# Performance work log

Measured on AMD Instinct MI355X. Metric: run time of the kernel, lower is better.

## Reference

```python
import jax, jax.numpy as jnp
import numpy as np

GRID = 128            # hardcoded in NeRFRenderer.__init__
BOUND = 4.0           # cfg.bound
CASCADE = 3           # 1 + ceil(log2(BOUND))
N_CELLS = GRID ** 3
N_CAMS = 32


def _part1by2(x):
    # interleave bits of a 10-bit int with two zero bits (instant-ngp morton3D)
    x = x & 0x000003FF
    x = (x | (x << 16)) & 0x030000FF
    x = (x | (x << 8)) & 0x0300F00F
    x = (x | (x << 4)) & 0x030C30C3
    x = (x | (x << 2)) & 0x09249249
    return x


def _morton3d(coords):
    # coords: [N,3] int32 -> [N] int32 morton codes (x lowest bit)
    x = _part1by2(coords[:, 0])
    y = _part1by2(coords[:, 1])
    z = _part1by2(coords[:, 2])
    return x | (y << 1) | (z << 2)


def setup_inputs() -> dict:
    key = jax.random.key(0)
    k1, k2 = jax.random.split(key)
    density_grid = jax.random.uniform(k1, (CASCADE, N_CELLS), dtype=jnp.float32)
    poses = jax.random.normal(k2, (N_CAMS, 4, 4), dtype=jnp.float32)
    # fx, fy, cx, cy for a 512x512 pinhole camera
    intrinsics = jnp.array([1111.1, 1111.1, 256.0, 256.0], dtype=jnp.float32)
    return {"density_grid": density_grid, "poses": poses, "intrinsics": intrinsics}


def reference(density_grid, poses, intrinsics):
    # Faithful vectorized mark_untrained_grid: for every grid cell and cascade,
    # test aabb containment and visibility in any camera frustum, then scatter
    # -1 into density_grid at the morton-encoded cell index where untrained.
    fx, fy, cx, cy = intrinsics[0], intrinsics[1], intrinsics[2], intrinsics[3]
    g = jnp.arange(GRID, dtype=jnp.int32)
    xx, yy, zz = jnp.meshgrid(g, g, g, indexing="ij")
    coords = jnp.stack([xx.ravel(), yy.ravel(), zz.ravel()], axis=-1)  # [N,3]
    indices = _morton3d(coords)                                        # [N] permutation of 0..N-1
    world = 2.0 * coords.astype(jnp.float32) / (GRID - 1) - 1.0        # [N,3] in [-1,1]

    R = poses[:, :3, :3]   # [B,3,3]
    t = poses[:, :3, 3]    # [B,3]

    new_grid = []
    for cas in range(CASCADE):
        bnd = min(2.0 ** cas, BOUND)
        h = bnd / GRID                       # half_grid_size
        cxyz = world * (bnd - h)             # [N,3] cascade world coords

        in_aabb = jnp.all(cxyz >= (-BOUND - h), axis=-1) & \
                  jnp.all(cxyz <= (BOUND + h), axis=-1)          # [N]

        # cam_xyzs = (cxyz - t[b]) @ R[b]  -> [B,N,3]
        cam = jnp.einsum("nj,bjk->bnk", cxyz, R) - jnp.einsum("bj,bjk->bk", t, R)[:, None, :]
        mask_z = cam[..., 2] > 0
        mask_x = jnp.abs(cam[..., 0]) < (cx / fx) * cam[..., 2] + 2.0 * h
        mask_y = jnp.abs(cam[..., 1]) < (cy / fy) * cam[..., 2] + 2.0 * h
        visible = jnp.any(mask_z & mask_x & mask_y, axis=0)      # [N]

        untrained = (~in_aabb) | (~visible)                      # [N] in coord order
        mark = jnp.zeros((N_CELLS,), dtype=bool).at[indices].set(untrained)  # morton scatter
        new_grid.append(jnp.where(mark, jnp.float32(-1.0), density_grid[cas]))

    return jnp.stack(new_grid, axis=0)
```

## Files before the change

kernel.cpp:

```cpp
#include <hip/hip_runtime.h>
#include <stdint.h>


constexpr int GRIDN  = 128;
constexpr int NCELLS = GRIDN * GRIDN * GRIDN;
constexpr int NCAMS  = 32;
constexpr int BLOCK  = 256;
constexpr int CPB    = BLOCK * 8;

__device__ __forceinline__ uint32_t compact1by2(uint32_t x) {
    x &= 0x09249249u;
    x = (x ^ (x >> 2))  & 0x030c30c3u;
    x = (x ^ (x >> 4))  & 0x0300f00fu;
    x = (x ^ (x >> 8))  & 0x030000ffu;
    x = (x ^ (x >> 16)) & 0x000003ffu;
    return x;
}

__launch_bounds__(BLOCK)
__global__ void nerf_mark_kernel(const float* __restrict__ dg,
                                 const float* __restrict__ poses,
                                 const float* __restrict__ intr,
                                 float* __restrict__ out) {
    __shared__ __align__(16) float sRd[NCAMS * 12];
    __shared__ float sc0[GRIDN];
    __shared__ float sax[2];

    constexpr float S0  = 1.0f - 1.0f / 128.0f;
    constexpr float T0  = 2.0f / 128.0f, T1 = 4.0f / 128.0f, T2 = 8.0f / 128.0f;
    constexpr float PAD = 1e-3f;

    const int tid = threadIdx.x;
    for (int i = tid; i < NCAMS * 12; i += BLOCK) {
        int b = i / 12, k = i - b * 12;
        const float* P = poses + b * 16;
        if (k < 9) {
            sRd[i] = P[(k / 3) * 4 + (k % 3)];
        } else {
            int kk = k - 9;
            sRd[i] = fmaf(P[11], P[8 + kk], fmaf(P[7], P[4 + kk], P[3] * P[kk]));
        }
    }
    if (tid < GRIDN) {
        float w = (2.0f * (float)tid) / 127.0f - 1.0f;
        sc0[tid] = __fmul_rn(w, S0);
    }
    if (tid == 0) { sax[0] = intr[2] / intr[0]; sax[1] = intr[3] / intr[1]; }
    __syncthreads();

    const int lane = tid & 63;
    const uint32_t wbase = (uint32_t)blockIdx.x * CPB + ((uint32_t)(tid >> 6)) * 512u;

    const int xi = ((lane & 1) << 1) | (((lane >> 3) & 1) << 2);
    const int yi = (((lane >> 1) & 1) << 1) | (((lane >> 4) & 1) << 2);
    const int zi = (((lane >> 2) & 1) << 1) | (((lane >> 5) & 1) << 2);
    const int X0 = compact1by2(wbase);
    const int Y0 = compact1by2(wbase >> 1);
    const int Z0 = compact1by2(wbase >> 2);
    const float cxv[2] = { sc0[X0 + xi], sc0[X0 + xi + 1] };
    const float cyv[2] = { sc0[Y0 + yi], sc0[Y0 + yi + 1] };
    const float czv[2] = { sc0[Z0 + zi], sc0[Z0 + zi + 1] };
    const float ax = sax[0], ay = sax[1];

    const float gxl = sc0[X0], gxh = sc0[X0 + 7];
    const float gyl = sc0[Y0], gyh = sc0[Y0 + 7];
    const float gzl = sc0[Z0], gzh = sc0[Z0 + 7];
    const float gcx = 0.5f * (gxl + gxh), ghx = 0.5f * (gxh - gxl);
    const float gcy = 0.5f * (gyl + gyh), ghy = 0.5f * (gyh - gyl);
    const float gcz = 0.5f * (gzl + gzh), ghz = 0.5f * (gzh - gzl);

    const int cb = lane & 31;
    bool po0, in0, po1, in1, po2, in2;
    {
        const float4* A = reinterpret_cast<const float4*>(&sRd[cb * 12]);
        const float4 qa = A[0], qb = A[1], qc = A[2];
        const float ddx = qc.y, ddy = qc.z, ddz = qc.w;
        const float pcx = fmaf(gcz, qb.z, fmaf(gcy, qa.w, gcx * qa.x));
        const float pcy = fmaf(gcz, qb.w, fmaf(gcy, qb.x, gcx * qa.y));
        const float pcz = fmaf(gcz, qc.x, fmaf(gcy, qb.y, gcx * qa.z));
        const float F1 = fmaf(ax, pcz, -pcx), F2 = fmaf(ax, pcz, pcx);
        const float F3 = fmaf(ay, pcz, -pcy), F4 = fmaf(ay, pcz, pcy);
        const float r0 = fmaf(ghz, fabsf(qc.x), fmaf(ghy, fabsf(qb.y), ghx * fabsf(qa.z)));
        const float a1x = fmaf(ax, qa.z, -qa.x), a1y = fmaf(ax, qb.y, -qa.w), a1z = fmaf(ax, qc.x, -qb.z);
        const float a2x = fmaf(ax, qa.z,  qa.x), a2y = fmaf(ax, qb.y,  qa.w), a2z = fmaf(ax, qc.x,  qb.z);
        const float a3x = fmaf(ay, qa.z, -qa.y), a3y = fmaf(ay, qb.y, -qb.x), a3z = fmaf(ay, qc.x, -qb.w);
        const float a4x = fmaf(ay, qa.z,  qa.y), a4y = fmaf(ay, qb.y,  qb.x), a4z = fmaf(ay, qc.x,  qb.w);
        const float r1 = fmaf(ghz, fabsf(a1z), fmaf(ghy, fabsf(a1y), ghx * fabsf(a1x)));
        const float r2 = fmaf(ghz, fabsf(a2z), fmaf(ghy, fabsf(a2y), ghx * fabsf(a2x)));
        const float r3 = fmaf(ghz, fabsf(a3z), fmaf(ghy, fabsf(a3y), ghx * fabsf(a3x)));
        const float r4 = fmaf(ghz, fabsf(a4z), fmaf(ghy, fabsf(a4y), ghx * fabsf(a4x)));
        const float e1 = fmaf(ax, ddz, -ddx), e2 = fmaf(ax, ddz, ddx);
        const float e3 = fmaf(ay, ddz, -ddy), e4 = fmaf(ay, ddz, ddy);

        auto classify = [&](float s, float T, bool& poss, bool& allin) {
            const float v0 = fmaf(s, pcz, -ddz);
            const float v1 = fmaf(s, F1, T - e1);
            const float v2 = fmaf(s, F2, T - e2);
            const float v3 = fmaf(s, F3, T - e3);
            const float v4 = fmaf(s, F4, T - e4);
            const float m0h = fmaf(s, r0, v0), m0l = fmaf(-s, r0, v0);
            const float m1h = fmaf(s, r1, v1), m1l = fmaf(-s, r1, v1);
            const float m2h = fmaf(s, r2, v2), m2l = fmaf(-s, r2, v2);
            const float m3h = fmaf(s, r3, v3), m3l = fmaf(-s, r3, v3);
            const float m4h = fmaf(s, r4, v4), m4l = fmaf(-s, r4, v4);
            poss  = !((m0h <= -PAD) | (m1h <= -PAD) | (m2h <= -PAD)
                                    | (m3h <= -PAD) | (m4h <= -PAD));
            allin = (m0l >= PAD) & (m1l >= PAD) & (m2l >= PAD)
                                 & (m3l >= PAD) & (m4l >= PAD);
        };
        classify(1.0f, T0, po0, in0);
        classify(2.0f, T1, po1, in1);
        classify(4.0f, T2, po2, in2);
    }

    const uint32_t allin0 = (uint32_t)__ballot(in0);
    const uint32_t allin1 = (uint32_t)__ballot(in1);
    const uint32_t allin2 = (uint32_t)__ballot(in2);
    const uint32_t poss0  = (uint32_t)__ballot(po0);
    const uint32_t poss1  = (uint32_t)__ballot(po1);
    const uint32_t poss2  = (uint32_t)__ballot(po2);

    const bool sat0 = (allin0 != 0u), sat1 = (allin1 != 0u), sat2 = (allin2 != 0u);
    bool v0[8], v1[8], v2[8];
    #pragma unroll
    for (int s = 0; s < 8; ++s) { v0[s] = sat0; v1[s] = sat1; v2[s] = sat2; }

    const uint32_t u0 = sat0 ? 0u : poss0;
    const uint32_t u1 = sat1 ? 0u : poss1;
    const uint32_t u2 = sat2 ? 0u : poss2;
    uint32_t u = u0 | u1 | u2;
    while (u) {
        const int b = __ffs(u) - 1;
        const uint32_t bit = 1u << b;
        u &= u - 1;
        const float4* B = reinterpret_cast<const float4*>(&sRd[b * 12]);
        const float4 qa = B[0], qb = B[1], qc = B[2];

        float p0[8], p1[8], p2[8];
        #pragma unroll
        for (int x = 0; x < 2; ++x) {
            const float i0 = cxv[x] * qa.x;
            const float i1 = cxv[x] * qa.y;
            const float i2 = cxv[x] * qa.z;
            #pragma unroll
            for (int y = 0; y < 2; ++y) {
                const float j0 = fmaf(cyv[y], qa.w, i0);
                const float j1 = fmaf(cyv[y], qb.x, i1);
                const float j2 = fmaf(cyv[y], qb.y, i2);
                #pragma unroll
                for (int z = 0; z < 2; ++z) {
                    const int s = x + 2 * y + 4 * z;
                    p0[s] = fmaf(czv[z], qb.z, j0);
                    p1[s] = fmaf(czv[z], qb.w, j1);
                    p2[s] = fmaf(czv[z], qc.x, j2);
                }
            }
        }

        if (u0 & bit) {
            #pragma unroll
            for (int s = 0; s < 8; ++s) {
                const float zz = __fsub_rn(p2[s], qc.w);
                const float xx = __fsub_rn(p0[s], qc.y);
                const float yy = __fsub_rn(p1[s], qc.z);
                v0[s] = v0[s] | ((zz > 0.0f)
                              & (fabsf(xx) < __fadd_rn(__fmul_rn(ax, zz), T0))
                              & (fabsf(yy) < __fadd_rn(__fmul_rn(ay, zz), T0)));
            }
        }
        if (u1 & bit) {
            #pragma unroll
            for (int s = 0; s < 8; ++s) {
                const float zz = fmaf(2.0f, p2[s], -qc.w);
                const float xx = fmaf(2.0f, p0[s], -qc.y);
                const float yy = fmaf(2.0f, p1[s], -qc.z);
                v1[s] = v1[s] | ((zz > 0.0f)
                              & (fabsf(xx) < __fadd_rn(__fmul_rn(ax, zz), T1))
                              & (fabsf(yy) < __fadd_rn(__fmul_rn(ay, zz), T1)));
            }
        }
        if (u2 & bit) {
            #pragma unroll
            for (int s = 0; s < 8; ++s) {
                const float zz = fmaf(4.0f, p2[s], -qc.w);
                const float xx = fmaf(4.0f, p0[s], -qc.y);
                const float yy = fmaf(4.0f, p1[s], -qc.z);
                v2[s] = v2[s] | ((zz > 0.0f)
                              & (fabsf(xx) < __fadd_rn(__fmul_rn(ax, zz), T2))
                              & (fabsf(yy) < __fadd_rn(__fmul_rn(ay, zz), T2)));
            }
        }

        bool allv = true;
        #pragma unroll
        for (int s = 0; s < 8; ++s) allv = allv & v0[s] & v1[s] & v2[s];
        if (__all(allv)) break;
    }

    const int mA = (int)(wbase + 8u * (uint32_t)lane);
    #pragma unroll
    for (int cas = 0; cas < 3; ++cas) {
        const bool* v = (cas == 0) ? v0 : (cas == 1) ? v1 : v2;
        const float* src = dg + cas * NCELLS + mA;
        float* dst = out + cas * NCELLS + mA;
        const float4 dlo = *reinterpret_cast<const float4*>(src);
        const float4 dhi = *reinterpret_cast<const float4*>(src + 4);
        float4 olo, ohi;
        olo.x = v[0] ? dlo.x : -1.0f; olo.y = v[1] ? dlo.y : -1.0f;
        olo.z = v[2] ? dlo.z : -1.0f; olo.w = v[3] ? dlo.w : -1.0f;
        ohi.x = v[4] ? dhi.x : -1.0f; ohi.y = v[5] ? dhi.y : -1.0f;
        ohi.z = v[6] ? dhi.z : -1.0f; ohi.w = v[7] ? dhi.w : -1.0f;
        *reinterpret_cast<float4*>(dst)     = olo;
        *reinterpret_cast<float4*>(dst + 4) = ohi;
    }
}

extern "C" void kernel_launch(void* const* d_in, const int* in_sizes, int n_in,
                              void* d_out, int out_size, void* d_ws, size_t ws_size,
                              hipStream_t stream) {
    const float* dg    = (const float*)d_in[0];
    const float* poses = (const float*)d_in[1];
    const float* intr  = (const float*)d_in[2];
    float* out = (float*)d_out;

    nerf_mark_kernel<<<NCELLS / CPB, BLOCK, 0, stream>>>(dg, poses, intr, out);
}
```

Baseline: 15.74 us.

## Process 16 cells per thread with per-cascade early exit and skip reads for fully-untrained waves

Doubles the cells per thread to 16 (4x2x2 sub-block) and halves the grid, so the wave-level frustum culling covers 16x8x8 bricks. Visibility flags become bitmasks, and each cascade now retires its own camera set independently instead of waiting for all three. When a wave's cascade is entirely untrained, the density-grid read is skipped and -1 is stored directly. The trade-offs are fewer waves for latency hiding, looser brick bounds that let more cameras pass culling, and extra per-camera ballots.

Measured after the change: 21.74 us. +38.1%, slower.

```diff
diff --git a/kernel.cpp b/kernel.cpp
--- a/kernel.cpp
+++ b/kernel.cpp
@@ -6,7 +6,7 @@
 constexpr int NCELLS = GRIDN * GRIDN * GRIDN;
 constexpr int NCAMS  = 32;
 constexpr int BLOCK  = 256;
-constexpr int CPB    = BLOCK * 8;
+constexpr int CPB    = BLOCK * 16;
 
 __device__ __forceinline__ uint32_t compact1by2(uint32_t x) {
     x &= 0x09249249u;
@@ -49,20 +49,20 @@
     __syncthreads();
 
     const int lane = tid & 63;
-    const uint32_t wbase = (uint32_t)blockIdx.x * CPB + ((uint32_t)(tid >> 6)) * 512u;
-
-    const int xi = ((lane & 1) << 1) | (((lane >> 3) & 1) << 2);
-    const int yi = (((lane >> 1) & 1) << 1) | (((lane >> 4) & 1) << 2);
-    const int zi = (((lane >> 2) & 1) << 1) | (((lane >> 5) & 1) << 2);
+    const uint32_t wbase = (uint32_t)blockIdx.x * CPB + ((uint32_t)(tid >> 6)) * 1024u;
+
+    const int xi = (((lane >> 2) & 1) << 2) | (((lane >> 5) & 1) << 3);
+    const int yi = ((lane & 1) << 1) | (((lane >> 3) & 1) << 2);
+    const int zi = (((lane >> 1) & 1) << 1) | (((lane >> 4) & 1) << 2);
     const int X0 = compact1by2(wbase);
     const int Y0 = compact1by2(wbase >> 1);
     const int Z0 = compact1by2(wbase >> 2);
-    const float cxv[2] = { sc0[X0 + xi], sc0[X0 + xi + 1] };
+    const float cxv[4] = { sc0[X0 + xi], sc0[X0 + xi + 1], sc0[X0 + xi + 2], sc0[X0 + xi + 3] };
     const float cyv[2] = { sc0[Y0 + yi], sc0[Y0 + yi + 1] };
     const float czv[2] = { sc0[Z0 + zi], sc0[Z0 + zi + 1] };
     const float ax = sax[0], ay = sax[1];
 
-    const float gxl = sc0[X0], gxh = sc0[X0 + 7];
+    const float gxl = sc0[X0], gxh = sc0[X0 + 15];
     const float gyl = sc0[Y0], gyh = sc0[Y0 + 7];
     const float gzl = sc0[Z0], gzh = sc0[Z0 + 7];
     const float gcx = 0.5f * (gxl + gxh), ghx = 0.5f * (gxh - gxl);
@@ -93,16 +93,16 @@
         const float e3 = fmaf(ay, ddz, -ddy), e4 = fmaf(ay, ddz, ddy);
 
         auto classify = [&](float s, float T, bool& poss, bool& allin) {
-            const float v0 = fmaf(s, pcz, -ddz);
-            const float v1 = fmaf(s, F1, T - e1);
-            const float v2 = fmaf(s, F2, T - e2);
-            const float v3 = fmaf(s, F3, T - e3);
-            const float v4 = fmaf(s, F4, T - e4);
-            const float m0h = fmaf(s, r0, v0), m0l = fmaf(-s, r0, v0);
-            const float m1h = fmaf(s, r1, v1), m1l = fmaf(-s, r1, v1);
-            const float m2h = fmaf(s, r2, v2), m2l = fmaf(-s, r2, v2);
-            const float m3h = fmaf(s, r3, v3), m3l = fmaf(-s, r3, v3);
-            const float m4h = fmaf(s, r4, v4), m4l = fmaf(-s, r4, v4);
+            const float w0 = fmaf(s, pcz, -ddz);
+            const float w1 = fmaf(s, F1, T - e1);
+            const float w2 = fmaf(s, F2, T - e2);
+            const float w3 = fmaf(s, F3, T - e3);
+            const float w4 = fmaf(s, F4, T - e4);
+            const float m0h = fmaf(s, r0, w0), m0l = fmaf(-s, r0, w0);
+            const float m1h = fmaf(s, r1, w1), m1l = fmaf(-s, r1, w1);
+            const float m2h = fmaf(s, r2, w2), m2l = fmaf(-s, r2, w2);
+            const float m3h = fmaf(s, r3, w3), m3l = fmaf(-s, r3, w3);
+            const float m4h = fmaf(s, r4, w4), m4l = fmaf(-s, r4, w4);
             poss  = !((m0h <= -PAD) | (m1h <= -PAD) | (m2h <= -PAD)
                                     | (m3h <= -PAD) | (m4h <= -PAD));
             allin = (m0l >= PAD) & (m1l >= PAD) & (m2l >= PAD)
@@ -121,9 +121,10 @@
     const uint32_t poss2  = (uint32_t)__ballot(po2);
 
     const bool sat0 = (allin0 != 0u), sat1 = (allin1 != 0u), sat2 = (allin2 != 0u);
-    bool v0[8], v1[8], v2[8];
-    #pragma unroll
-    for (int s = 0; s < 8; ++s) { v0[s] = sat0; v1[s] = sat1; v2[s] = sat2; }
+    uint32_t v0m = sat0 ? 0xffffu : 0u;
+    uint32_t v1m = sat1 ? 0xffffu : 0u;
+    uint32_t v2m = sat2 ? 0xffffu : 0u;
+    bool d0 = sat0, d1 = sat1, d2 = sat2;
 
     const uint32_t u0 = sat0 ? 0u : poss0;
     const uint32_t u1 = sat1 ? 0u : poss1;
@@ -135,83 +136,87 @@
         u &= u - 1;
         const float4* B = reinterpret_cast<const float4*>(&sRd[b * 12]);
         const float4 qa = B[0], qb = B[1], qc = B[2];
-
-        float p0[8], p1[8], p2[8];
+        const bool t0 = ((u0 & bit) != 0u) & !d0;
+        const bool t1 = ((u1 & bit) != 0u) & !d1;
+        const bool t2 = ((u2 & bit) != 0u) & !d2;
+
         #pragma unroll
-        for (int x = 0; x < 2; ++x) {
-            const float i0 = cxv[x] * qa.x;
-            const float i1 = cxv[x] * qa.y;
-            const float i2 = cxv[x] * qa.z;
+        for (int xo = 0; xo < 4; ++xo) {
+            const float i0 = cxv[xo] * qa.x;
+            const float i1 = cxv[xo] * qa.y;
+            const float i2 = cxv[xo] * qa.z;
             #pragma unroll
-            for (int y = 0; y < 2; ++y) {
-                const float j0 = fmaf(cyv[y], qa.w, i0);
-                const float j1 = fmaf(cyv[y], qb.x, i1);
-                const float j2 = fmaf(cyv[y], qb.y, i2);
+            for (int yo = 0; yo < 2; ++yo) {
+                const float j0 = fmaf(cyv[yo], qa.w, i0);
+                const float j1 = fmaf(cyv[yo], qb.x, i1);
+                const float j2 = fmaf(cyv[yo], qb.y, i2);
                 #pragma unroll
-                for (int z = 0; z < 2; ++z) {
-                    const int s = x + 2 * y + 4 * z;
-                    p0[s] = fmaf(czv[z], qb.z, j0);
-                    p1[s] = fmaf(czv[z], qb.w, j1);
-                    p2[s] = fmaf(czv[z], qc.x, j2);
+                for (int zo = 0; zo < 2; ++zo) {
+                    const int s = (xo & 1) + 8 * (xo >> 1) + 2 * yo + 4 * zo;
+                    const uint32_t bs = 1u << s;
+                    const float p0 = fmaf(czv[zo], qb.z, j0);
+                    const float p1 = fmaf(czv[zo], qb.w, j1);
+                    const float p2 = fmaf(czv[zo], qc.x, j2);
+                    if (t0) {
+                        const float zz = __fsub_rn(p2, qc.w);
+                        const float xx = __fsub_rn(p0, qc.y);
+                        const float yy = __fsub_rn(p1, qc.z);
+                        const bool c = (zz > 0.0f)
+                                     & (fabsf(xx) < __fadd_rn(__fmul_rn(ax, zz), T0))
+                                     & (fabsf(yy) < __fadd_rn(__fmul_rn(ay, zz), T0));
+                        v0m |= c ? bs : 0u;
+                    }
+                    if (t1) {
+                        const float zz = fmaf(2.0f, p2, -qc.w);
+                        const float xx = fmaf(2.0f, p0, -qc.y);
+                        const float yy = fmaf(2.0f, p1, -qc.z);
+                        const bool c = (zz > 0.0f)
+                                     & (fabsf(xx) < __fadd_rn(__fmul_rn(ax, zz), T1))
+                                     & (fabsf(yy) < __fadd_rn(__fmul_rn(ay, zz), T1));
+                        v1m |= c ? bs : 0u;
+                    }
+                    if (t2) {
+                        const float zz = fmaf(4.0f, p2, -qc.w);
+                        const float xx = fmaf(4.0f, p0, -qc.y);
+                        const float yy = fmaf(4.0f, p1, -qc.z);
+                        const bool c = (zz > 0.0f)
+                                     & (fabsf(xx) < __fadd_rn(__fmul_rn(ax, zz), T2))
+                                     & (fabsf(yy) < __fadd_rn(__fmul_rn(ay, zz), T2));
+                        v2m |= c ? bs : 0u;
+                    }
                 }
             }
         }
 
-        if (u0 & bit) {
-            #pragma unroll
-            for (int s = 0; s < 8; ++s) {
-                const float zz = __fsub_rn(p2[s], qc.w);
-                const float xx = __fsub_rn(p0[s], qc.y);
-                const float yy = __fsub_rn(p1[s], qc.z);
-                v0[s] = v0[s] | ((zz > 0.0f)
-                              & (fabsf(xx) < __fadd_rn(__fmul_rn(ax, zz), T0))
-                              & (fabsf(yy) < __fadd_rn(__fmul_rn(ay, zz), T0)));
-            }
-        }
-        if (u1 & bit) {
-            #pragma unroll
-            for (int s = 0; s < 8; ++s) {
-                const float zz = fmaf(2.0f, p2[s], -qc.w);
-                const float xx = fmaf(2.0f, p0[s], -qc.y);
-                const float yy = fmaf(2.0f, p1[s], -qc.z);
-                v1[s] = v1[s] | ((zz > 0.0f)
-                              & (fabsf(xx) < __fadd_rn(__fmul_rn(ax, zz), T1))
-                              & (fabsf(yy) < __fadd_rn(__fmul_rn(ay, zz), T1)));
-            }
-        }
-        if (u2 & bit) {
-            #pragma unroll
-            for (int s = 0; s < 8; ++s) {
-                const float zz = fmaf(4.0f, p2[s], -qc.w);
-                const float xx = fmaf(4.0f, p0[s], -qc.y);
-                const float yy = fmaf(4.0f, p1[s], -qc.z);
-                v2[s] = v2[s] | ((zz > 0.0f)
-                              & (fabsf(xx) < __fadd_rn(__fmul_rn(ax, zz), T2))
-                              & (fabsf(yy) < __fadd_rn(__fmul_rn(ay, zz), T2)));
-            }
-        }
-
-        bool allv = true;
-        #pragma unroll
-        for (int s = 0; s < 8; ++s) allv = allv & v0[s] & v1[s] & v2[s];
-        if (__all(allv)) break;
-    }
-
-    const int mA = (int)(wbase + 8u * (uint32_t)lane);
+        if (t0) d0 = __all(v0m == 0xffffu);
+        if (t1) d1 = __all(v1m == 0xffffu);
+        if (t2) d2 = __all(v2m == 0xffffu);
+        u &= (d0 ? 0u : u0) | (d1 ? 0u : u1) | (d2 ? 0u : u2);
+    }
+
+    const int mA = (int)(wbase + 16u * (uint32_t)lane);
     #pragma unroll
     for (int cas = 0; cas < 3; ++cas) {
-        const bool* v = (cas == 0) ? v0 : (cas == 1) ? v1 : v2;
+        const uint32_t vm = (cas == 0) ? v0m : (cas == 1) ? v1m : v2m;
         const float* src = dg + cas * NCELLS + mA;
         float* dst = out + cas * NCELLS + mA;
-        const float4 dlo = *reinterpret_cast<const float4*>(src);
-        const float4 dhi = *reinterpret_cast<const float4*>(src + 4);
-        float4 olo, ohi;
-        olo.x = v[0] ? dlo.x : -1.0f; olo.y = v[1] ? dlo.y : -1.0f;
-        olo.z = v[2] ? dlo.z : -1.0f; olo.w = v[3] ? dlo.w : -1.0f;
-        ohi.x = v[4] ? dhi.x : -1.0f; ohi.y = v[5] ? dhi.y : -1.0f;
-        ohi.z = v[6] ? dhi.z : -1.0f; ohi.w = v[7] ? dhi.w : -1.0f;
-        *reinterpret_cast<float4*>(dst)     = olo;
-        *reinterpret_cast<float4*>(dst + 4) = ohi;
+        if (__any(vm != 0u)) {
+            #pragma unroll
+            for (int g = 0; g < 4; ++g) {
+                const float4 d = *reinterpret_cast<const float4*>(src + 4 * g);
+                float4 o;
+                o.x = (vm & (1u << (4 * g + 0))) ? d.x : -1.0f;
+                o.y = (vm & (1u << (4 * g + 1))) ? d.y : -1.0f;
+                o.z = (vm & (1u << (4 * g + 2))) ? d.z : -1.0f;
+                o.w = (vm & (1u << (4 * g + 3))) ? d.w : -1.0f;
+                *reinterpret_cast<float4*>(dst + 4 * g) = o;
+            }
+        } else {
+            const float4 neg = make_float4(-1.0f, -1.0f, -1.0f, -1.0f);
+            #pragma unroll
+            for (int g = 0; g < 4; ++g)
+                *reinterpret_cast<float4*>(dst + 4 * g) = neg;
+        }
     }
 }
 
```
